# Performance work log

Hardware: AMD Instinct MI355X
Metric: run time of the kernel (lower is better)

The kernel has to match this reference:

```python
import jax, jax.numpy as jnp
import numpy as np

N = 2048
IN_C, HID, LAT = 128, 128, 64
E_SPARSE = 65536


def gcn_conv(x, W, b, src, dst, w, n):
    # PyG GCNConv: h = D^-1/2 (A+I) D^-1/2 (x W) + b  (self-loops already in edge list)
    deg = jax.ops.segment_sum(w, dst, num_segments=n)
    dinv = jnp.where(deg > 0, jax.lax.rsqrt(deg), 0.0)
    norm = dinv[src] * w * dinv[dst]            # [E]
    h = x @ W                                   # [N, out]
    agg = jax.ops.segment_sum(h[src] * norm[:, None], dst, num_segments=n)
    return agg + b


def setup_inputs() -> dict:
    key = jax.random.key(0)
    ks = jax.random.split(key, 9)
    x = jax.random.normal(ks[0], (N, IN_C), jnp.float32)
    masked_y = jax.random.normal(ks[1], (N, N), jnp.float32)
    edge_index = jax.random.randint(ks[2], (2, E_SPARSE), 0, N, dtype=jnp.int32)
    s = 0.05
    W1 = jax.random.normal(ks[3], (IN_C, HID), jnp.float32) * s
    b1 = jnp.zeros((HID,), jnp.float32)
    Wmu = jax.random.normal(ks[4], (HID, LAT), jnp.float32) * s
    bmu = jnp.zeros((LAT,), jnp.float32)
    Wls = jax.random.normal(ks[5], (HID, LAT), jnp.float32) * s
    bls = jnp.zeros((LAT,), jnp.float32)
    return {"x": x, "masked_y": masked_y, "W1": W1, "b1": b1,
            "Wmu": Wmu, "bmu": bmu, "Wls": Wls, "bls": bls,
            "edge_index": edge_index}


def reference(x, masked_y, W1, b1, Wmu, bmu, Wls, bls, edge_index):
    n = x.shape[0]
    half = n // 2
    # masking leaves only the top-left [half, half] block of masked_y nonzero;
    # dense_to_sparse on that block -> all half*half (row, col) pairs (entries != 0 a.s.)
    rows = jnp.repeat(jnp.arange(half, dtype=edge_index.dtype), half)
    cols = jnp.tile(jnp.arange(half, dtype=edge_index.dtype), half)
    y_w = jax.nn.sigmoid(masked_y[:half, :half].reshape(-1))
    loop = jnp.arange(n, dtype=edge_index.dtype)
    src = jnp.concatenate([edge_index[0], rows, loop])
    dst = jnp.concatenate([edge_index[1], cols, loop])
    w = jnp.concatenate([jnp.ones((edge_index.shape[1],), x.dtype), y_w,
                         jnp.ones((n,), x.dtype)])
    hidden = jax.nn.relu(gcn_conv(x, W1, b1, src, dst, w, n))
    z_mu = gcn_conv(hidden, Wmu, bmu, src, dst, w, n)
    z_logstd = gcn_conv(hidden, Wls, bls, src, dst, w, n)
    return (z_mu, z_logstd)
```

## Files before the change

kernel.cpp:

```cpp
#include <hip/hip_runtime.h>

#define NN 2048
#define HALF 1024
#define CC 128
#define EE 65536
#define CAP 128

typedef unsigned short u16;

__device__ __forceinline__ float sigm(float v){ return 1.0f/(1.0f + __expf(-v)); }

__device__ __forceinline__ float dinv_lo(int i, const int* __restrict__ cnt,
                                         const float* __restrict__ colsum){
  return rsqrtf(1.0f + (float)cnt[i] + colsum[i]);
}
__device__ __forceinline__ float dinv_any(int i, const int* __restrict__ cnt,
                                          const float* __restrict__ colsum){
  float cs = (i < HALF) ? colsum[i] : 0.0f;
  return rsqrtf(1.0f + (float)cnt[i] + cs);
}

__global__ __launch_bounds__(256) void k_prep(
    const float* __restrict__ my, const int* __restrict__ ei, const float* __restrict__ x,
    const float* __restrict__ W1,
    const float* __restrict__ bmu, const float* __restrict__ bls,
    float* __restrict__ SpRaw, float* __restrict__ colsum,
    int* __restrict__ cnt, u16* __restrict__ bucket, float* __restrict__ H0,
    float* __restrict__ AGG1, float* __restrict__ out)
{
  __shared__ float la[8][CC];
  int b = blockIdx.x, t = threadIdx.x;
  int gid = b*256 + t;
  if (gid < 65536) {
    ((float4*)AGG1)[gid] = make_float4(0.f,0.f,0.f,0.f);
  } else if (gid < 131072) {
    int i = gid - 65536;
    int g4 = (i & 15)*4;
    const float* bb = (i < 32768) ? bmu : bls;
    ((float4*)out)[i] = make_float4(bb[g4], bb[g4+1], bb[g4+2], bb[g4+3]);
  }

  if (b < 128) {
    int c0 = t*4;
    float cs0=0.f, cs1=0.f, cs2=0.f, cs3=0.f;
    #pragma unroll 2
    for (int rr=0; rr<8; ++rr){
      int r = b*8 + rr;
      float4 v = *(const float4*)(my + (size_t)r*NN + c0);
      float s0=sigm(v.x), s1=sigm(v.y), s2=sigm(v.z), s3=sigm(v.w);
      *(float4*)(SpRaw + (size_t)r*HALF + c0) = make_float4(s0,s1,s2,s3);
      cs0+=s0; cs1+=s1; cs2+=s2; cs3+=s3;
    }
    atomicAdd(&colsum[c0+0], cs0);
    atomicAdd(&colsum[c0+1], cs1);
    atomicAdd(&colsum[c0+2], cs2);
    atomicAdd(&colsum[c0+3], cs3);
  } else if (b < 384) {
    int e = (b-128)*256 + t;
    int s = ei[e], d = ei[EE + e];
    int slot = atomicAdd(&cnt[d], 1);
    if (slot < CAP) bucket[d*CAP + slot] = (u16)s;
  } else {
    int row0 = (b-384)*8;
    #pragma unroll
    for (int i=0;i<4;i++){
      int idx = i*256 + t;
      la[idx>>7][idx&127] = x[(size_t)row0*CC + idx];
    }
    __syncthreads();
    int f = t & 127, rh = t >> 7;
    const float4* a0 = (const float4*)la[rh*4+0];
    const float4* a1 = (const float4*)la[rh*4+1];
    const float4* a2 = (const float4*)la[rh*4+2];
    const float4* a3 = (const float4*)la[rh*4+3];
    float o0=0.f, o1=0.f, o2=0.f, o3=0.f;
    #pragma unroll 4
    for (int k4=0;k4<32;k4++){
      float4 v0=a0[k4], v1=a1[k4], v2=a2[k4], v3=a3[k4];
      float w0 = W1[(k4*4+0)*CC + f];
      float w1 = W1[(k4*4+1)*CC + f];
      float w2 = W1[(k4*4+2)*CC + f];
      float w3 = W1[(k4*4+3)*CC + f];
      o0=fmaf(v0.x,w0,o0); o0=fmaf(v0.y,w1,o0); o0=fmaf(v0.z,w2,o0); o0=fmaf(v0.w,w3,o0);
      o1=fmaf(v1.x,w0,o1); o1=fmaf(v1.y,w1,o1); o1=fmaf(v1.z,w2,o1); o1=fmaf(v1.w,w3,o1);
      o2=fmaf(v2.x,w0,o2); o2=fmaf(v2.y,w1,o2); o2=fmaf(v2.z,w2,o2); o2=fmaf(v2.w,w3,o2);
      o3=fmaf(v3.x,w0,o3); o3=fmaf(v3.y,w1,o3); o3=fmaf(v3.z,w2,o3); o3=fmaf(v3.w,w3,o3);
    }
    H0[(size_t)(row0 + rh*4 + 0)*CC + f] = o0;
    H0[(size_t)(row0 + rh*4 + 1)*CC + f] = o1;
    H0[(size_t)(row0 + rh*4 + 2)*CC + f] = o2;
    H0[(size_t)(row0 + rh*4 + 3)*CC + f] = o3;
  }
}

__global__ __launch_bounds__(256) void k_layer1(
  const float* __restrict__ SpRaw, const float* __restrict__ F,
  const int* __restrict__ cnt, const float* __restrict__ colsum,
  const u16* __restrict__ bucket, float* __restrict__ AGG)
{
  __shared__ float sdinv[NN];
  int b = blockIdx.x, t = threadIdx.x;
  #pragma unroll
  for (int i=0;i<8;i++){
    int j = i*256 + t;
    float cs = (j < HALF) ? colsum[j] : 0.0f;
    sdinv[j] = rsqrtf(1.0f + (float)cnt[j] + cs);
  }
  __syncthreads();
  int lane = t & 63, f0 = lane*2;
  if (b < 256) {
    int dbase = (b>>2)*16 + (t>>6)*4;
    int r0 = (b&3)*256;
    float a00=0.f,a01=0.f,a10=0.f,a11=0.f,a20=0.f,a21=0.f,a30=0.f,a31=0.f;
    #pragma unroll 4
    for (int rr=0; rr<256; ++rr){
      int r = r0 + rr;
      float2 fv = *(const float2*)(F + (size_t)r*CC + f0);
      float sc = sdinv[r];
      float fx = fv.x*sc, fy = fv.y*sc;
      float4 s4 = *(const float4*)(SpRaw + (size_t)r*HALF + dbase);
      a00=fmaf(s4.x,fx,a00); a01=fmaf(s4.x,fy,a01);
      a10=fmaf(s4.y,fx,a10); a11=fmaf(s4.y,fy,a11);
      a20=fmaf(s4.z,fx,a20); a21=fmaf(s4.z,fy,a21);
      a30=fmaf(s4.w,fx,a30); a31=fmaf(s4.w,fy,a31);
    }
    float d0=sdinv[dbase+0], d1=sdinv[dbase+1], d2=sdinv[dbase+2], d3=sdinv[dbase+3];
    float* o = AGG + (size_t)dbase*CC + f0;
    atomicAdd(o + 0*CC + 0, a00*d0); atomicAdd(o + 0*CC + 1, a01*d0);
    atomicAdd(o + 1*CC + 0, a10*d1); atomicAdd(o + 1*CC + 1, a11*d1);
    atomicAdd(o + 2*CC + 0, a20*d2); atomicAdd(o + 2*CC + 1, a21*d2);
    atomicAdd(o + 3*CC + 0, a30*d3); atomicAdd(o + 3*CC + 1, a31*d3);
  } else {
    int d = (b-256)*4 + (t>>6);
    float dd = sdinv[d];
    float2 sv = *(const float2*)(F + (size_t)d*CC + f0);
    float ax = dd*sv.x, ay = dd*sv.y;
    int m = cnt[d]; m = m > CAP ? CAP : m;
    const u16* bk = bucket + d*CAP;
    int j = 0;
    for (; j+1 < m; j += 2){
      unsigned pr = *(const unsigned*)(bk + j);
      int s0 = pr & 0xffff, s1 = pr >> 16;
      float w0 = sdinv[s0], w1 = sdinv[s1];
      float2 v0 = *(const float2*)(F + (size_t)s0*CC + f0);
      float2 v1 = *(const float2*)(F + (size_t)s1*CC + f0);
      ax = fmaf(w0, v0.x, ax); ay = fmaf(w0, v0.y, ay);
      ax = fmaf(w1, v1.x, ax); ay = fmaf(w1, v1.y, ay);
    }
    if (j < m){
      int s0 = bk[j];
      float w0 = sdinv[s0];
      float2 v0 = *(const float2*)(F + (size_t)s0*CC + f0);
      ax = fmaf(w0, v0.x, ax); ay = fmaf(w0, v0.y, ay);
    }
    atomicAdd(&AGG[(size_t)d*CC + f0    ], dd*ax);
    atomicAdd(&AGG[(size_t)d*CC + f0 + 1], dd*ay);
  }
}

__global__ __launch_bounds__(256) void k_mid(
  const float* __restrict__ AGG1, const float* __restrict__ b1,
  const float* __restrict__ Wmu, const float* __restrict__ Wls,
  const int* __restrict__ cnt, const float* __restrict__ colsum,
  float* __restrict__ G)
{
  __shared__ float la[8][CC];
  int b = blockIdx.x, t = threadIdx.x;
  int row0 = b*8;
  #pragma unroll
  for (int i=0;i<4;i++){
    int idx = i*256 + t;
    float v = AGG1[(size_t)row0*CC + idx] + b1[idx & 127];
    la[idx>>7][idx&127] = v > 0.f ? v : 0.f;
  }
  __syncthreads();
  int f = t & 127, rh = t >> 7;
  int g = f & 63;
  const float* W = (f < 64) ? Wmu : Wls;
  const float4* a0 = (const float4*)la[rh*4+0];
  const float4* a1 = (const float4*)la[rh*4+1];
  const float4* a2 = (const float4*)la[rh*4+2];
  const float4* a3 = (const float4*)la[rh*4+3];
  float o0=0.f, o1=0.f, o2=0.f, o3=0.f;
  #pragma unroll 4
  for (int k4=0;k4<32;k4++){
    float4 v0=a0[k4], v1=a1[k4], v2=a2[k4], v3=a3[k4];
    float w0 = W[(k4*4+0)*64 + g];
    float w1 = W[(k4*4+1)*64 + g];
    float w2 = W[(k4*4+2)*64 + g];
    float w3 = W[(k4*4+3)*64 + g];
    o0=fmaf(v0.x,w0,o0); o0=fmaf(v0.y,w1,o0); o0=fmaf(v0.z,w2,o0); o0=fmaf(v0.w,w3,o0);
    o1=fmaf(v1.x,w0,o1); o1=fmaf(v1.y,w1,o1); o1=fmaf(v1.z,w2,o1); o1=fmaf(v1.w,w3,o1);
    o2=fmaf(v2.x,w0,o2); o2=fmaf(v2.y,w1,o2); o2=fmaf(v2.z,w2,o2); o2=fmaf(v2.w,w3,o2);
    o3=fmaf(v3.x,w0,o3); o3=fmaf(v3.y,w1,o3); o3=fmaf(v3.z,w2,o3); o3=fmaf(v3.w,w3,o3);
  }
  {
    int row = row0 + rh*4 + 0; G[(size_t)row*CC + f] = o0 * dinv_any(row, cnt, colsum);
  }
  { int row = row0 + rh*4 + 1; G[(size_t)row*CC + f] = o1 * dinv_any(row, cnt, colsum); }
  { int row = row0 + rh*4 + 2; G[(size_t)row*CC + f] = o2 * dinv_any(row, cnt, colsum); }
  { int row = row0 + rh*4 + 3; G[(size_t)row*CC + f] = o3 * dinv_any(row, cnt, colsum); }
}

__global__ __launch_bounds__(256) void k_layer2(
  const float* __restrict__ SpRaw, const float* __restrict__ G,
  const int* __restrict__ cnt, const float* __restrict__ colsum,
  const u16* __restrict__ bucket, float* __restrict__ out)
{
  int b = blockIdx.x, t = threadIdx.x;
  int lane = t & 63, f0 = lane*2;
  size_t obase = (f0 < 64) ? 0 : (size_t)NN*64;
  int g0 = f0 & 63;
  if (b < 256) {
    int dbase = (b>>2)*16 + (t>>6)*4;
    int r0 = (b&3)*256;
    float a00=0.f,a01=0.f,a10=0.f,a11=0.f,a20=0.f,a21=0.f,a30=0.f,a31=0.f;
    #pragma unroll 4
    for (int rr=0; rr<256; ++rr){
      int r = r0 + rr;
      float2 gv = *(const float2*)(G + (size_t)r*CC + f0);
      float4 s4 = *(const float4*)(SpRaw + (size_t)r*HALF + dbase);
      a00=fmaf(s4.x,gv.x,a00); a01=fmaf(s4.x,gv.y,a01);
      a10=fmaf(s4.y,gv.x,a10); a11=fmaf(s4.y,gv.y,a11);
      a20=fmaf(s4.z,gv.x,a20); a21=fmaf(s4.z,gv.y,a21);
      a30=fmaf(s4.w,gv.x,a30); a31=fmaf(s4.w,gv.y,a31);
    }
    float d0=dinv_lo(dbase+0,cnt,colsum), d1=dinv_lo(dbase+1,cnt,colsum);
    float d2=dinv_lo(dbase+2,cnt,colsum), d3=dinv_lo(dbase+3,cnt,colsum);
    float* o = out + obase + (size_t)dbase*64 + g0;
    atomicAdd(o + 0*64 + 0, a00*d0); atomicAdd(o + 0*64 + 1, a01*d0);
    atomicAdd(o + 1*64 + 0, a10*d1); atomicAdd(o + 1*64 + 1, a11*d1);
    atomicAdd(o + 2*64 + 0, a20*d2); atomicAdd(o + 2*64 + 1, a21*d2);
    atomicAdd(o + 3*64 + 0, a30*d3); atomicAdd(o + 3*64 + 1, a31*d3);
  } else {
    int d = (b-256)*4 + (t>>6);
    float2 a = *(const float2*)(G + (size_t)d*CC + f0);
    float ax = a.x, ay = a.y;
    int m = cnt[d]; m = m > CAP ? CAP : m;
    const u16* bk = bucket + d*CAP;
    int j = 0;
    for (; j+1 < m; j += 2){
      unsigned pr = *(const unsigned*)(bk + j);
      int s0 = pr & 0xffff, s1 = pr >> 16;
      float2 v0 = *(const float2*)(G + (size_t)s0*CC + f0);
      float2 v1 = *(const float2*)(G + (size_t)s1*CC + f0);
      ax += v0.x + v1.x; ay += v0.y + v1.y;
    }
    if (j < m){
      int s0 = bk[j];
      float2 v0 = *(const float2*)(G + (size_t)s0*CC + f0);
      ax += v0.x; ay += v0.y;
    }
    float dd = dinv_any(d, cnt, colsum);
    atomicAdd(&out[obase + (size_t)d*64 + g0    ], dd*ax);
    atomicAdd(&out[obase + (size_t)d*64 + g0 + 1], dd*ay);
  }
}

extern "C" void kernel_launch(void* const* d_in, const int* in_sizes, int n_in,
                              void* d_out, int out_size, void* d_ws, size_t ws_size,
                              hipStream_t stream)
{
  (void)in_sizes; (void)n_in; (void)out_size; (void)ws_size;
  const float* x   = (const float*)d_in[0];
  const float* my  = (const float*)d_in[1];
  const float* W1  = (const float*)d_in[2];
  const float* b1  = (const float*)d_in[3];
  const float* Wmu = (const float*)d_in[4];
  const float* bmu = (const float*)d_in[5];
  const float* Wls = (const float*)d_in[6];
  const float* bls = (const float*)d_in[7];
  const int*   ei  = (const int*)d_in[8];
  float* out = (float*)d_out;
  char* ws = (char*)d_ws;

  int*   cnt    = (int*)  (ws + 0);
  float* colsum = (float*)(ws + 8192);
  float* AGG1   = (float*)(ws + 12288);
  u16*   bucket = (u16*)  (ws + 1060864);
  float* SpRaw  = (float*)(ws + 1585152);
  float* H0     = (float*)(ws + 5779456);
  float* G      = (float*)(ws + 6828032);

  hipMemsetAsync(ws, 0, 12288, stream);
  k_prep  <<<640, 256, 0, stream>>>(my, ei, x, W1, bmu, bls,
                                    SpRaw, colsum, cnt, bucket, H0, AGG1, out);
  k_layer1<<<768, 256, 0, stream>>>(SpRaw, H0, cnt, colsum, bucket, AGG1);
  k_mid   <<<256, 256, 0, stream>>>(AGG1, b1, Wmu, Wls, cnt, colsum, G);
  k_layer2<<<768, 256, 0, stream>>>(SpRaw, G, cnt, colsum, bucket, out);
}
```

Baseline: 162.0 us.

## Fuse all GCN stages into one cooperative kernel with grid syncs

Replaces the four separate launches (prep, layer1, mid, layer2) with a single cooperative kernel of 512 blocks that separates the stages with grid.sync(). Float atomicAdd accumulation into AGG and out is replaced by writing per-chunk partial buffers (DP for the dense block, SP for the sparse part) that the next stage sums, so the zero-init and bias-fill passes go away. The sparse gather now handles two destinations per wavefront with float4 loads. This removes launch gaps and atomic contention, but grid-wide barriers have their own cost and the dense stages now run on fewer blocks.

Result: slower. 408.9 us (+152.4%).

```diff
diff --git a/kernel.cpp b/kernel.cpp
--- a/kernel.cpp
+++ b/kernel.cpp
@@ -1,4 +1,7 @@
 #include <hip/hip_runtime.h>
+#include <hip/hip_cooperative_groups.h>
+
+namespace cg = cooperative_groups;
 
 #define NN 2048
 #define HALF 1024
@@ -10,35 +13,21 @@
 
 __device__ __forceinline__ float sigm(float v){ return 1.0f/(1.0f + __expf(-v)); }
 
-__device__ __forceinline__ float dinv_lo(int i, const int* __restrict__ cnt,
-                                         const float* __restrict__ colsum){
-  return rsqrtf(1.0f + (float)cnt[i] + colsum[i]);
-}
-__device__ __forceinline__ float dinv_any(int i, const int* __restrict__ cnt,
-                                          const float* __restrict__ colsum){
-  float cs = (i < HALF) ? colsum[i] : 0.0f;
-  return rsqrtf(1.0f + (float)cnt[i] + cs);
-}
-
-__global__ __launch_bounds__(256) void k_prep(
+__global__ __launch_bounds__(256) void k_fused(
     const float* __restrict__ my, const int* __restrict__ ei, const float* __restrict__ x,
-    const float* __restrict__ W1,
-    const float* __restrict__ bmu, const float* __restrict__ bls,
+    const float* __restrict__ W1, const float* __restrict__ b1,
+    const float* __restrict__ Wmu, const float* __restrict__ bmu,
+    const float* __restrict__ Wls, const float* __restrict__ bls,
     float* __restrict__ SpRaw, float* __restrict__ colsum,
-    int* __restrict__ cnt, u16* __restrict__ bucket, float* __restrict__ H0,
-    float* __restrict__ AGG1, float* __restrict__ out)
+    int* __restrict__ cnt, u16* __restrict__ bucket,
+    float* __restrict__ H0, float* __restrict__ Gm,
+    float* __restrict__ SP, float* __restrict__ DP,
+    float* __restrict__ out)
 {
+  __shared__ float sdinv[NN];
   __shared__ float la[8][CC];
+  cg::grid_group grid = cg::this_grid();
   int b = blockIdx.x, t = threadIdx.x;
-  int gid = b*256 + t;
-  if (gid < 65536) {
-    ((float4*)AGG1)[gid] = make_float4(0.f,0.f,0.f,0.f);
-  } else if (gid < 131072) {
-    int i = gid - 65536;
-    int g4 = (i & 15)*4;
-    const float* bb = (i < 32768) ? bmu : bls;
-    ((float4*)out)[i] = make_float4(bb[g4], bb[g4+1], bb[g4+2], bb[g4+3]);
-  }
 
   if (b < 128) {
     int c0 = t*4;
@@ -55,13 +44,17 @@
     atomicAdd(&colsum[c0+1], cs1);
     atomicAdd(&colsum[c0+2], cs2);
     atomicAdd(&colsum[c0+3], cs3);
-  } else if (b < 384) {
-    int e = (b-128)*256 + t;
-    int s = ei[e], d = ei[EE + e];
-    int slot = atomicAdd(&cnt[d], 1);
-    if (slot < CAP) bucket[d*CAP + slot] = (u16)s;
+  } else if (b < 256) {
+    int e0 = (b-128)*512 + t;
+    #pragma unroll
+    for (int i=0;i<2;i++){
+      int e = e0 + i*256;
+      int s = ei[e], d = ei[EE + e];
+      int slot = atomicAdd(&cnt[d], 1);
+      if (slot < CAP) bucket[d*CAP + slot] = (u16)s;
+    }
   } else {
-    int row0 = (b-384)*8;
+    int row0 = (b-256)*8;
     #pragma unroll
     for (int i=0;i<4;i++){
       int idx = i*256 + t;
@@ -91,15 +84,8 @@
     H0[(size_t)(row0 + rh*4 + 2)*CC + f] = o2;
     H0[(size_t)(row0 + rh*4 + 3)*CC + f] = o3;
   }
-}
-
-__global__ __launch_bounds__(256) void k_layer1(
-  const float* __restrict__ SpRaw, const float* __restrict__ F,
-  const int* __restrict__ cnt, const float* __restrict__ colsum,
-  const u16* __restrict__ bucket, float* __restrict__ AGG)
-{
-  __shared__ float sdinv[NN];
-  int b = blockIdx.x, t = threadIdx.x;
+  grid.sync();
+
   #pragma unroll
   for (int i=0;i<8;i++){
     int j = i*256 + t;
@@ -107,15 +93,17 @@
     sdinv[j] = rsqrtf(1.0f + (float)cnt[j] + cs);
   }
   __syncthreads();
-  int lane = t & 63, f0 = lane*2;
+
   if (b < 256) {
+    int lane = t & 63, f0 = lane*2;
     int dbase = (b>>2)*16 + (t>>6)*4;
-    int r0 = (b&3)*256;
+    int chunk = b & 3;
+    int r0 = chunk*256;
     float a00=0.f,a01=0.f,a10=0.f,a11=0.f,a20=0.f,a21=0.f,a30=0.f,a31=0.f;
     #pragma unroll 4
     for (int rr=0; rr<256; ++rr){
       int r = r0 + rr;
-      float2 fv = *(const float2*)(F + (size_t)r*CC + f0);
+      float2 fv = *(const float2*)(H0 + (size_t)r*CC + f0);
       float sc = sdinv[r];
       float fx = fv.x*sc, fy = fv.y*sc;
       float4 s4 = *(const float4*)(SpRaw + (size_t)r*HALF + dbase);
@@ -125,16 +113,18 @@
       a30=fmaf(s4.w,fx,a30); a31=fmaf(s4.w,fy,a31);
     }
     float d0=sdinv[dbase+0], d1=sdinv[dbase+1], d2=sdinv[dbase+2], d3=sdinv[dbase+3];
-    float* o = AGG + (size_t)dbase*CC + f0;
-    atomicAdd(o + 0*CC + 0, a00*d0); atomicAdd(o + 0*CC + 1, a01*d0);
-    atomicAdd(o + 1*CC + 0, a10*d1); atomicAdd(o + 1*CC + 1, a11*d1);
-    atomicAdd(o + 2*CC + 0, a20*d2); atomicAdd(o + 2*CC + 1, a21*d2);
-    atomicAdd(o + 3*CC + 0, a30*d3); atomicAdd(o + 3*CC + 1, a31*d3);
+    float* o = DP + ((size_t)chunk*HALF + dbase)*CC + f0;
+    o[0*CC+0]=a00*d0; o[0*CC+1]=a01*d0;
+    o[1*CC+0]=a10*d1; o[1*CC+1]=a11*d1;
+    o[2*CC+0]=a20*d2; o[2*CC+1]=a21*d2;
+    o[3*CC+0]=a30*d3; o[3*CC+1]=a31*d3;
   } else {
-    int d = (b-256)*4 + (t>>6);
+    int w = t>>6, hw = (t>>5)&1, l = t&31;
+    int d = (b-256)*8 + w*2 + hw;
+    int f0 = l*4;
     float dd = sdinv[d];
-    float2 sv = *(const float2*)(F + (size_t)d*CC + f0);
-    float ax = dd*sv.x, ay = dd*sv.y;
+    float4 sv = *(const float4*)(H0 + (size_t)d*CC + f0);
+    float ax=dd*sv.x, ay=dd*sv.y, az=dd*sv.z, aw=dd*sv.w;
     int m = cnt[d]; m = m > CAP ? CAP : m;
     const u16* bk = bucket + d*CAP;
     int j = 0;
@@ -142,118 +132,124 @@
       unsigned pr = *(const unsigned*)(bk + j);
       int s0 = pr & 0xffff, s1 = pr >> 16;
       float w0 = sdinv[s0], w1 = sdinv[s1];
-      float2 v0 = *(const float2*)(F + (size_t)s0*CC + f0);
-      float2 v1 = *(const float2*)(F + (size_t)s1*CC + f0);
-      ax = fmaf(w0, v0.x, ax); ay = fmaf(w0, v0.y, ay);
-      ax = fmaf(w1, v1.x, ax); ay = fmaf(w1, v1.y, ay);
+      float4 v0 = *(const float4*)(H0 + (size_t)s0*CC + f0);
+      float4 v1 = *(const float4*)(H0 + (size_t)s1*CC + f0);
+      ax=fmaf(w0,v0.x,ax); ay=fmaf(w0,v0.y,ay); az=fmaf(w0,v0.z,az); aw=fmaf(w0,v0.w,aw);
+      ax=fmaf(w1,v1.x,ax); ay=fmaf(w1,v1.y,ay); az=fmaf(w1,v1.z,az); aw=fmaf(w1,v1.w,aw);
     }
     if (j < m){
       int s0 = bk[j];
       float w0 = sdinv[s0];
-      float2 v0 = *(const float2*)(F + (size_t)s0*CC + f0);
-      ax = fmaf(w0, v0.x, ax); ay = fmaf(w0, v0.y, ay);
-    }
-    atomicAdd(&AGG[(size_t)d*CC + f0    ], dd*ax);
-    atomicAdd(&AGG[(size_t)d*CC + f0 + 1], dd*ay);
-  }
-}
-
-__global__ __launch_bounds__(256) void k_mid(
-  const float* __restrict__ AGG1, const float* __restrict__ b1,
-  const float* __restrict__ Wmu, const float* __restrict__ Wls,
-  const int* __restrict__ cnt, const float* __restrict__ colsum,
-  float* __restrict__ G)
-{
-  __shared__ float la[8][CC];
-  int b = blockIdx.x, t = threadIdx.x;
-  int row0 = b*8;
-  #pragma unroll
-  for (int i=0;i<4;i++){
-    int idx = i*256 + t;
-    float v = AGG1[(size_t)row0*CC + idx] + b1[idx & 127];
-    la[idx>>7][idx&127] = v > 0.f ? v : 0.f;
-  }
-  __syncthreads();
-  int f = t & 127, rh = t >> 7;
-  int g = f & 63;
-  const float* W = (f < 64) ? Wmu : Wls;
-  const float4* a0 = (const float4*)la[rh*4+0];
-  const float4* a1 = (const float4*)la[rh*4+1];
-  const float4* a2 = (const float4*)la[rh*4+2];
-  const float4* a3 = (const float4*)la[rh*4+3];
-  float o0=0.f, o1=0.f, o2=0.f, o3=0.f;
-  #pragma unroll 4
-  for (int k4=0;k4<32;k4++){
-    float4 v0=a0[k4], v1=a1[k4], v2=a2[k4], v3=a3[k4];
-    float w0 = W[(k4*4+0)*64 + g];
-    float w1 = W[(k4*4+1)*64 + g];
-    float w2 = W[(k4*4+2)*64 + g];
-    float w3 = W[(k4*4+3)*64 + g];
-    o0=fmaf(v0.x,w0,o0); o0=fmaf(v0.y,w1,o0); o0=fmaf(v0.z,w2,o0); o0=fmaf(v0.w,w3,o0);
-    o1=fmaf(v1.x,w0,o1); o1=fmaf(v1.y,w1,o1); o1=fmaf(v1.z,w2,o1); o1=fmaf(v1.w,w3,o1);
-    o2=fmaf(v2.x,w0,o2); o2=fmaf(v2.y,w1,o2); o2=fmaf(v2.z,w2,o2); o2=fmaf(v2.w,w3,o2);
-    o3=fmaf(v3.x,w0,o3); o3=fmaf(v3.y,w1,o3); o3=fmaf(v3.z,w2,o3); o3=fmaf(v3.w,w3,o3);
-  }
+      float4 v0 = *(const float4*)(H0 + (size_t)s0*CC + f0);
+      ax=fmaf(w0,v0.x,ax); ay=fmaf(w0,v0.y,ay); az=fmaf(w0,v0.z,az); aw=fmaf(w0,v0.w,aw);
+    }
+    *(float4*)(SP + (size_t)d*CC + f0) = make_float4(dd*ax, dd*ay, dd*az, dd*aw);
+  }
+  grid.sync();
+
   {
-    int row = row0 + rh*4 + 0; G[(size_t)row*CC + f] = o0 * dinv_any(row, cnt, colsum);
-  }
-  { int row = row0 + rh*4 + 1; G[(size_t)row*CC + f] = o1 * dinv_any(row, cnt, colsum); }
-  { int row = row0 + rh*4 + 2; G[(size_t)row*CC + f] = o2 * dinv_any(row, cnt, colsum); }
-  { int row = row0 + rh*4 + 3; G[(size_t)row*CC + f] = o3 * dinv_any(row, cnt, colsum); }
-}
-
-__global__ __launch_bounds__(256) void k_layer2(
-  const float* __restrict__ SpRaw, const float* __restrict__ G,
-  const int* __restrict__ cnt, const float* __restrict__ colsum,
-  const u16* __restrict__ bucket, float* __restrict__ out)
-{
-  int b = blockIdx.x, t = threadIdx.x;
-  int lane = t & 63, f0 = lane*2;
-  size_t obase = (f0 < 64) ? 0 : (size_t)NN*64;
-  int g0 = f0 & 63;
+    int row0 = b*4;
+    #pragma unroll
+    for (int i=0;i<2;i++){
+      int idx = i*256 + t;
+      int r = row0 + (idx>>7), c = idx & 127;
+      float v = SP[(size_t)r*CC + c];
+      if (row0 < HALF)
+        v += DP[((size_t)0*HALF + r)*CC + c] + DP[((size_t)1*HALF + r)*CC + c]
+           + DP[((size_t)2*HALF + r)*CC + c] + DP[((size_t)3*HALF + r)*CC + c];
+      v += b1[c];
+      la[idx>>7][c] = v > 0.f ? v : 0.f;
+    }
+    __syncthreads();
+    int f = t & 127, rh = t >> 7, g = f & 63;
+    const float* W = (f < 64) ? Wmu : Wls;
+    const float4* a0 = (const float4*)la[rh*2+0];
+    const float4* a1 = (const float4*)la[rh*2+1];
+    float o0=0.f, o1=0.f;
+    #pragma unroll 4
+    for (int k4=0;k4<32;k4++){
+      float4 v0=a0[k4], v1=a1[k4];
+      float w0 = W[(k4*4+0)*64 + g];
+      float w1 = W[(k4*4+1)*64 + g];
+      float w2 = W[(k4*4+2)*64 + g];
+      float w3 = W[(k4*4+3)*64 + g];
+      o0=fmaf(v0.x,w0,o0); o0=fmaf(v0.y,w1,o0); o0=fmaf(v0.z,w2,o0); o0=fmaf(v0.w,w3,o0);
+      o1=fmaf(v1.x,w0,o1); o1=fmaf(v1.y,w1,o1); o1=fmaf(v1.z,w2,o1); o1=fmaf(v1.w,w3,o1);
+    }
+    int rA = row0 + rh*2;
+    Gm[(size_t)(rA+0)*CC + f] = o0 * sdinv[rA+0];
+    Gm[(size_t)(rA+1)*CC + f] = o1 * sdinv[rA+1];
+  }
+  grid.sync();
+
   if (b < 256) {
+    int lane = t & 63, f0 = lane*2;
     int dbase = (b>>2)*16 + (t>>6)*4;
-    int r0 = (b&3)*256;
+    int chunk = b & 3;
+    int r0 = chunk*256;
     float a00=0.f,a01=0.f,a10=0.f,a11=0.f,a20=0.f,a21=0.f,a30=0.f,a31=0.f;
     #pragma unroll 4
     for (int rr=0; rr<256; ++rr){
       int r = r0 + rr;
-      float2 gv = *(const float2*)(G + (size_t)r*CC + f0);
+      float2 gv = *(const float2*)(Gm + (size_t)r*CC + f0);
       float4 s4 = *(const float4*)(SpRaw + (size_t)r*HALF + dbase);
       a00=fmaf(s4.x,gv.x,a00); a01=fmaf(s4.x,gv.y,a01);
       a10=fmaf(s4.y,gv.x,a10); a11=fmaf(s4.y,gv.y,a11);
       a20=fmaf(s4.z,gv.x,a20); a21=fmaf(s4.z,gv.y,a21);
       a30=fmaf(s4.w,gv.x,a30); a31=fmaf(s4.w,gv.y,a31);
     }
-    float d0=dinv_lo(dbase+0,cnt,colsum), d1=dinv_lo(dbase+1,cnt,colsum);
-    float d2=dinv_lo(dbase+2,cnt,colsum), d3=dinv_lo(dbase+3,cnt,colsum);
-    float* o = out + obase + (size_t)dbase*64 + g0;
-    atomicAdd(o + 0*64 + 0, a00*d0); atomicAdd(o + 0*64 + 1, a01*d0);
-    atomicAdd(o + 1*64 + 0, a10*d1); atomicAdd(o + 1*64 + 1, a11*d1);
-    atomicAdd(o + 2*64 + 0, a20*d2); atomicAdd(o + 2*64 + 1, a21*d2);
-    atomicAdd(o + 3*64 + 0, a30*d3); atomicAdd(o + 3*64 + 1, a31*d3);
+    float d0=sdinv[dbase+0], d1=sdinv[dbase+1], d2=sdinv[dbase+2], d3=sdinv[dbase+3];
+    float* o = DP + ((size_t)chunk*HALF + dbase)*CC + f0;
+    o[0*CC+0]=a00*d0; o[0*CC+1]=a01*d0;
+    o[1*CC+0]=a10*d1; o[1*CC+1]=a11*d1;
+    o[2*CC+0]=a20*d2; o[2*CC+1]=a21*d2;
+    o[3*CC+0]=a30*d3; o[3*CC+1]=a31*d3;
   } else {
-    int d = (b-256)*4 + (t>>6);
-    float2 a = *(const float2*)(G + (size_t)d*CC + f0);
-    float ax = a.x, ay = a.y;
+    int w = t>>6, hw = (t>>5)&1, l = t&31;
+    int d = (b-256)*8 + w*2 + hw;
+    int f0 = l*4;
+    float dd = sdinv[d];
+    float4 a = *(const float4*)(Gm + (size_t)d*CC + f0);
+    float ax=a.x, ay=a.y, az=a.z, aw=a.w;
     int m = cnt[d]; m = m > CAP ? CAP : m;
     const u16* bk = bucket + d*CAP;
     int j = 0;
     for (; j+1 < m; j += 2){
       unsigned pr = *(const unsigned*)(bk + j);
       int s0 = pr & 0xffff, s1 = pr >> 16;
-      float2 v0 = *(const float2*)(G + (size_t)s0*CC + f0);
-      float2 v1 = *(const float2*)(G + (size_t)s1*CC + f0);
+      float4 v0 = *(const float4*)(Gm + (size_t)s0*CC + f0);
+      float4 v1 = *(const float4*)(Gm + (size_t)s1*CC + f0);
       ax += v0.x + v1.x; ay += v0.y + v1.y;
+      az += v0.z + v1.z; aw += v0.w + v1.w;
     }
     if (j < m){
       int s0 = bk[j];
-      float2 v0 = *(const float2*)(G + (size_t)s0*CC + f0);
-      ax += v0.x; ay += v0.y;
-    }
-    float dd = dinv_any(d, cnt, colsum);
-    atomicAdd(&out[obase + (size_t)d*64 + g0    ], dd*ax);
-    atomicAdd(&out[obase + (size_t)d*64 + g0 + 1], dd*ay);
+      float4 v0 = *(const float4*)(Gm + (size_t)s0*CC + f0);
+      ax += v0.x; ay += v0.y; az += v0.z; aw += v0.w;
+    }
+    *(float4*)(SP + (size_t)d*CC + f0) = make_float4(dd*ax, dd*ay, dd*az, dd*aw);
+  }
+  grid.sync();
+
+  {
+    int tid = b*256 + t;
+    int half = tid >> 16;
+    int rem = tid & 65535;
+    int d = rem >> 5;
+    int g0 = (rem & 31)*2;
+    int f = g0 + (half << 6);
+    const float* bb = half ? bls : bmu;
+    float vx = bb[g0], vy = bb[g0+1];
+    const float* sp = SP + (size_t)d*CC + f;
+    vx += sp[0]; vy += sp[1];
+    if (d < HALF){
+      #pragma unroll
+      for (int k=0;k<4;k++){
+        const float* dp = DP + ((size_t)k*HALF + d)*CC + f;
+        vx += dp[0]; vy += dp[1];
+      }
+    }
+    *(float2*)(out + ((size_t)half*NN + d)*64 + g0) = make_float2(vx, vy);
   }
 }
 
@@ -276,16 +272,21 @@
 
   int*   cnt    = (int*)  (ws + 0);
   float* colsum = (float*)(ws + 8192);
-  float* AGG1   = (float*)(ws + 12288);
-  u16*   bucket = (u16*)  (ws + 1060864);
-  float* SpRaw  = (float*)(ws + 1585152);
-  float* H0     = (float*)(ws + 5779456);
-  float* G      = (float*)(ws + 6828032);
+  u16*   bucket = (u16*)  (ws + 12288);
+  float* SpRaw  = (float*)(ws + 536576);
+  float* H0     = (float*)(ws + 4730880);
+  float* Gm     = (float*)(ws + 5779456);
+  float* SP     = (float*)(ws + 6828032);
+  float* DP     = (float*)(ws + 7876608);
 
   hipMemsetAsync(ws, 0, 12288, stream);
-  k_prep  <<<640, 256, 0, stream>>>(my, ei, x, W1, bmu, bls,
-                                    SpRaw, colsum, cnt, bucket, H0, AGG1, out);
-  k_layer1<<<768, 256, 0, stream>>>(SpRaw, H0, cnt, colsum, bucket, AGG1);
-  k_mid   <<<256, 256, 0, stream>>>(AGG1, b1, Wmu, Wls, cnt, colsum, G);
-  k_layer2<<<768, 256, 0, stream>>>(SpRaw, G, cnt, colsum, bucket, out);
+
+  void* args[] = {
+    (void*)&my, (void*)&ei, (void*)&x, (void*)&W1, (void*)&b1,
+    (void*)&Wmu, (void*)&bmu, (void*)&Wls, (void*)&bls,
+    (void*)&SpRaw, (void*)&colsum, (void*)&cnt, (void*)&bucket,
+    (void*)&H0, (void*)&Gm, (void*)&SP, (void*)&DP, (void*)&out
+  };
+  hipLaunchCooperativeKernel(reinterpret_cast<const void*>(k_fused),
+                             dim3(512), dim3(256), args, 0, stream);
 }
```
